# Optimization experiments

Hardware: AMD Instinct MI355X
Metric: run time of the kernel (lower is better)

## Reference

```python
import jax, jax.numpy as jnp
import numpy as np

C = 1024      # channels
K = 7         # kernel_size
G = 1         # groups (G>1 crashes in the original torch code; see notes)
GC = C // G   # group_channels
OFFSET_SCALE = 2.0
LN_EPS = 1e-5


def setup_inputs() -> dict:
    key = jax.random.key(0)
    ks = jax.random.split(key, 8)
    N, L = 4, 2048
    s = 1.0 / np.sqrt(C)
    x = jax.random.normal(ks[0], (N, L, C), jnp.float32)
    Wi = jax.random.normal(ks[1], (C, C), jnp.float32) * s
    bi = jnp.zeros((C,), jnp.float32)
    dw_w = jax.random.normal(ks[2], (C, 1, 3), jnp.float32) * 0.5   # depthwise conv kernel (O, I/g=1, W)
    dw_b = jnp.zeros((C,), jnp.float32)
    ln_g = jnp.ones((C,), jnp.float32)
    ln_b = jnp.zeros((C,), jnp.float32)
    Wo = jax.random.normal(ks[3], (G * K, C), jnp.float32) * 0.02   # offset head (nonzero to exercise gather)
    bo = jnp.zeros((G * K,), jnp.float32)
    Wm = jax.random.normal(ks[4], (G * K, C), jnp.float32) * 0.02   # mask head
    bm = jnp.zeros((G * K,), jnp.float32)
    Wout = jax.random.normal(ks[5], (C, C), jnp.float32) * s
    bout = jnp.zeros((C,), jnp.float32)
    return {"x": x, "Wi": Wi, "bi": bi, "dw_w": dw_w, "dw_b": dw_b,
            "ln_g": ln_g, "ln_b": ln_b, "Wo": Wo, "bo": bo,
            "Wm": Wm, "bm": bm, "Wout": Wout, "bout": bout}


def _forward(x, Wi, bi, dw_w, dw_b, ln_g, ln_b, Wo, bo, Wm, bm, Wout, bout):
    N, L, Cc = x.shape
    dt = x.dtype
    # input projection
    x_proj = x @ Wi.T + bi                                  # [N,L,C]
    # depthwise conv (k=3, pad=1, groups=C) -> LayerNorm(C) -> GELU(exact)
    y = jax.lax.conv_general_dilated(
        x.transpose(0, 2, 1), dw_w, window_strides=(1,), padding=((1, 1),),
        dimension_numbers=("NCH", "OIH", "NCH"), feature_group_count=Cc)
    x_dw = y.transpose(0, 2, 1) + dw_b                       # [N,L,C]
    mu = x_dw.mean(-1, keepdims=True)
    var = ((x_dw - mu) ** 2).mean(-1, keepdims=True)
    x_dw = (x_dw - mu) * jax.lax.rsqrt(var + LN_EPS) * ln_g + ln_b
    x_dw = jax.nn.gelu(x_dw, approximate=False)
    # dynamic offsets and sampling mask
    offsets = (x_dw @ Wo.T + bo).reshape(N, L, G, K) * OFFSET_SCALE
    mask = jax.nn.softmax((x_dw @ Wm.T + bm).reshape(N, L, G, K), axis=-1)
    mask = jnp.nan_to_num(mask, nan=0.0)
    # absolute sampling positions
    ref_off = jnp.linspace(-(K // 2), K // 2, K).astype(dt)          # [K]
    pos = jnp.arange(L, dtype=dt)[None, :, None, None]               # [1,L,1,1]
    abs_pos = pos + ref_off[None, None, None, :] + offsets           # [N,L,G,K]
    apc = jnp.clip(abs_pos, 0.0, L - 1)
    p_floor = jnp.clip(apc.astype(jnp.int32), 0, L - 1)
    p_ceil = jnp.clip(p_floor + 1, 0, L - 1)
    w_ceil = apc - p_floor.astype(dt)
    w_floor = 1.0 - w_ceil
    valid = jnp.logical_not((abs_pos < 0) | (abs_pos > L - 1)).astype(dt)
    w_floor = w_floor * valid
    w_ceil = w_ceil * valid
    # gather + bilinear blend (G=1: each sample index grabs the full C channels)
    idx_f = p_floor.reshape(N, -1)[:, :, None]                       # [N, L*G*K, 1]
    idx_c = p_ceil.reshape(N, -1)[:, :, None]
    v_floor = jnp.take_along_axis(x_proj, idx_f, axis=1).reshape(N, L, G, K, GC)
    v_ceil = jnp.take_along_axis(x_proj, idx_c, axis=1).reshape(N, L, G, K, GC)
    sampled = v_floor * w_floor[..., None] + v_ceil * w_ceil[..., None]
    out = (sampled * mask[..., None]).sum(axis=3).reshape(N, L, Cc)  # sum over K
    return out @ Wout.T + bout


def reference(x, Wi, bi, dw_w, dw_b, ln_g, ln_b, Wo, bo, Wm, bm, Wout, bout):
    return _forward(x, Wi, bi, dw_w, dw_b, ln_g, ln_b, Wo, bo, Wm, bm, Wout, bout)
```

## Files before the change

kernel.cpp:

```cpp
#include <hip/hip_runtime.h>
#include <hip/hip_bf16.h>
#include <cstdint>

#define C_DIM 1024
#define L_DIM 2048
#define N_DIM 4
#define M_DIM (N_DIM * L_DIM)

typedef __attribute__((ext_vector_type(8))) short frag8;
typedef __attribute__((ext_vector_type(4)))  float f32x4;
typedef __attribute__((ext_vector_type(16))) float f32x16;

__device__ __forceinline__ void gl_lds16(const void* g, void* l) {
  __builtin_amdgcn_global_load_lds((const __attribute__((address_space(1))) void*)g,
                                   (__attribute__((address_space(3))) void*)l,
                                   16, 0, 0);
}
__device__ __forceinline__ void store_out(float* Y, size_t idx, float v) { Y[idx] = v; }
__device__ __forceinline__ void store_out(__hip_bfloat16* Y, size_t idx, float v) {
  Y[idx] = __float2bfloat16(v);
}
__device__ __forceinline__ float4 ldbf4(const __hip_bfloat16* p) {
  union { short4 s; __hip_bfloat16 h[4]; } u; u.s = *(const short4*)p;
  return make_float4((float)u.h[0], (float)u.h[1], (float)u.h[2], (float)u.h[3]);
}
__device__ __forceinline__ void stbf4(__hip_bfloat16* p, float4 v) {
  union { short4 s; __hip_bfloat16 h[4]; } u;
  u.h[0] = __float2bfloat16(v.x); u.h[1] = __float2bfloat16(v.y);
  u.h[2] = __float2bfloat16(v.z); u.h[3] = __float2bfloat16(v.w);
  *(short4*)p = u.s;
}
__device__ __forceinline__ float gelu_fast(float t) {
  const float t3 = t * t * t;
  const float ns = -1.5957691216f * t - 0.0713548163f * t3;
  return t / (1.f + __expf(ns));
}

__global__ __launch_bounds__(256)
void cvt_f32_bf16(const float* __restrict__ in, __hip_bfloat16* __restrict__ out, int n8) {
  const int i = blockIdx.x * 256 + threadIdx.x;
  if (i >= n8) return;
  const float4 a = *(const float4*)(in + (size_t)i * 8);
  const float4 b = *(const float4*)(in + (size_t)i * 8 + 4);
  union { __hip_bfloat16 h[8]; int4 q; } u;
  u.h[0] = __float2bfloat16(a.x); u.h[1] = __float2bfloat16(a.y);
  u.h[2] = __float2bfloat16(a.z); u.h[3] = __float2bfloat16(a.w);
  u.h[4] = __float2bfloat16(b.x); u.h[5] = __float2bfloat16(b.y);
  u.h[6] = __float2bfloat16(b.z); u.h[7] = __float2bfloat16(b.w);
  *(int4*)(out + (size_t)i * 8) = u.q;
}

template <typename TY>
__global__ __launch_bounds__(256, 2)
void gemm_db(const __hip_bfloat16* __restrict__ X,
             const __hip_bfloat16* __restrict__ W,
             const float* __restrict__ bias,
             TY* __restrict__ Y, int M, int N, int K)
{
  __shared__ __hip_bfloat16 As[2][2][128 * 32];
  __shared__ __hip_bfloat16 Bs[2][2][128 * 32];
  const int tid  = threadIdx.x;
  const int lane = tid & 63;
  const int wave = tid >> 6;
  const int bm = blockIdx.x * 128;
  const int bn = blockIdx.y * 128;
  const int wr = (wave >> 1) * 64;
  const int wc = (wave & 1) * 64;
  const int srow  = tid >> 2;
  const int skoff = (tid & 3) * 8;

  const __hip_bfloat16* gA0 = X + (size_t)(bm + srow) * K + skoff;
  const __hip_bfloat16* gA1 = X + (size_t)(bm + 64 + srow) * K + skoff;
  const __hip_bfloat16* gB0 = W + (size_t)(bn + srow) * K + skoff;
  const __hip_bfloat16* gB1 = W + (size_t)(bn + 64 + srow) * K + skoff;

  f32x16 acc[2][2] = {};
  const int arow  = lane & 31;
  const int akoff = (lane >> 5) * 8;

#define STAGE(k0, buf)                                        \
  do {                                                        \
    gl_lds16(gA0 + (k0),      &As[buf][0][tid * 8]);          \
    gl_lds16(gA1 + (k0),      &As[buf][0][2048 + tid * 8]);   \
    gl_lds16(gA0 + (k0) + 32, &As[buf][1][tid * 8]);          \
    gl_lds16(gA1 + (k0) + 32, &As[buf][1][2048 + tid * 8]);   \
    gl_lds16(gB0 + (k0),      &Bs[buf][0][tid * 8]);          \
    gl_lds16(gB1 + (k0),      &Bs[buf][0][2048 + tid * 8]);   \
    gl_lds16(gB0 + (k0) + 32, &Bs[buf][1][tid * 8]);          \
    gl_lds16(gB1 + (k0) + 32, &Bs[buf][1][2048 + tid * 8]);   \
  } while (0)

  STAGE(0, 0);
  __syncthreads();
  const int iters = K / 64;
  for (int it = 0; it < iters; ++it) {
    const int cur = it & 1;
    if (it + 1 < iters) STAGE((it + 1) * 64, cur ^ 1);

#pragma unroll
    for (int p = 0; p < 2; ++p)
#pragma unroll
      for (int h = 0; h < 2; ++h) {
        const frag8 a0 = *(const frag8*)&As[cur][p][(wr + arow) * 32 + h * 16 + akoff];
        const frag8 a1 = *(const frag8*)&As[cur][p][(wr + 32 + arow) * 32 + h * 16 + akoff];
        const frag8 b0 = *(const frag8*)&Bs[cur][p][(wc + arow) * 32 + h * 16 + akoff];
        const frag8 b1 = *(const frag8*)&Bs[cur][p][(wc + 32 + arow) * 32 + h * 16 + akoff];
        acc[0][0] = __builtin_amdgcn_mfma_f32_32x32x16_bf16(a0, b0, acc[0][0], 0, 0, 0);
        acc[0][1] = __builtin_amdgcn_mfma_f32_32x32x16_bf16(a0, b1, acc[0][1], 0, 0, 0);
        acc[1][0] = __builtin_amdgcn_mfma_f32_32x32x16_bf16(a1, b0, acc[1][0], 0, 0, 0);
        acc[1][1] = __builtin_amdgcn_mfma_f32_32x32x16_bf16(a1, b1, acc[1][1], 0, 0, 0);
      }
    __syncthreads();
  }
#undef STAGE

#pragma unroll
  for (int i = 0; i < 2; i++)
#pragma unroll
    for (int j = 0; j < 2; j++) {
      const int col = bn + wc + j * 32 + (lane & 31);
      const float bv = bias[col];
#pragma unroll
      for (int r = 0; r < 16; r++) {
        const int row = bm + wr + i * 32 + (r & 3) + 8 * (r >> 2) + 4 * (lane >> 5);
        store_out(Y, (size_t)row * N + col, acc[i][j][r] + bv);
      }
    }
}

struct Ld8f { float4 a, b; };
struct Ld8b { int4 a; };
__device__ __forceinline__ Ld8f ld8(const float* p) {
  return { *(const float4*)p, *(const float4*)(p + 4) };
}
__device__ __forceinline__ Ld8b ld8(const __hip_bfloat16* p) { return { *(const int4*)p }; }
__device__ __forceinline__ void st8(__hip_bfloat16* l, const Ld8f& v) {
  union { __hip_bfloat16 h[8]; int4 q; } u;
  u.h[0] = __float2bfloat16(v.a.x); u.h[1] = __float2bfloat16(v.a.y);
  u.h[2] = __float2bfloat16(v.a.z); u.h[3] = __float2bfloat16(v.a.w);
  u.h[4] = __float2bfloat16(v.b.x); u.h[5] = __float2bfloat16(v.b.y);
  u.h[6] = __float2bfloat16(v.b.z); u.h[7] = __float2bfloat16(v.b.w);
  *(int4*)l = u.q;
}
__device__ __forceinline__ void st8(__hip_bfloat16* l, const Ld8b& v) { *(int4*)l = v.a; }

template <typename TX, typename TY>
__global__ __launch_bounds__(256, 2)
void gemm_nt(const TX* __restrict__ X, const float* __restrict__ W,
             const float* __restrict__ bias, TY* __restrict__ Y, int M, int N, int K)
{
  __shared__ __hip_bfloat16 As[128 * 32];
  __shared__ __hip_bfloat16 Bs[128 * 32];
  const int tid  = threadIdx.x;
  const int lane = tid & 63;
  const int wave = tid >> 6;
  const int bm = blockIdx.x * 128;
  const int bn = blockIdx.y * 128;
  const int wr = (wave >> 1) * 64;
  const int wc = (wave & 1) * 64;
  const int srow  = tid >> 2;
  const int skoff = (tid & 3) * 8;

  f32x4 acc[4][4] = {};
  const TX*    gA0 = X + (size_t)(bm + srow) * K + skoff;
  const TX*    gA1 = X + (size_t)(bm + 64 + srow) * K + skoff;
  const float* gB0 = W + (size_t)(bn + srow) * K + skoff;
  const float* gB1 = W + (size_t)(bn + 64 + srow) * K + skoff;
  const int arow  = lane & 15;
  const int akoff = (lane >> 4) * 8;

  for (int k0 = 0; k0 < K; k0 += 32) {
    const auto va0 = ld8(gA0 + k0);
    const auto va1 = ld8(gA1 + k0);
    const auto vb0 = ld8(gB0 + k0);
    const auto vb1 = ld8(gB1 + k0);
    __syncthreads();
    st8(&As[srow * 32 + skoff],        va0);
    st8(&As[(64 + srow) * 32 + skoff], va1);
    st8(&Bs[srow * 32 + skoff],        vb0);
    st8(&Bs[(64 + srow) * 32 + skoff], vb1);
    __syncthreads();

    frag8 a[4], b[4];
#pragma unroll
    for (int i = 0; i < 4; i++)
      a[i] = *(const frag8*)&As[(wr + i * 16 + arow) * 32 + akoff];
#pragma unroll
    for (int j = 0; j < 4; j++)
      b[j] = *(const frag8*)&Bs[(wc + j * 16 + arow) * 32 + akoff];
#pragma unroll
    for (int i = 0; i < 4; i++)
#pragma unroll
      for (int j = 0; j < 4; j++)
        acc[i][j] = __builtin_amdgcn_mfma_f32_16x16x32_bf16(a[i], b[j], acc[i][j], 0, 0, 0);
  }
#pragma unroll
  for (int i = 0; i < 4; i++)
#pragma unroll
    for (int j = 0; j < 4; j++) {
      const int col = bn + wc + j * 16 + (lane & 15);
      const float bv = bias[col];
#pragma unroll
      for (int r = 0; r < 4; r++) {
        const int row = bm + wr + i * 16 + (lane >> 4) * 4 + r;
        store_out(Y, (size_t)row * N + col, acc[i][j][r] + bv);
      }
    }
}

__global__ __launch_bounds__(256)
void mid_fused_v4(const float* __restrict__ x,
                  const float* __restrict__ dw_w, const float* __restrict__ dw_b,
                  const float* __restrict__ ln_g, const float* __restrict__ ln_b,
                  const float* __restrict__ Wo,   const float* __restrict__ bo,
                  const float* __restrict__ Wm,   const float* __restrict__ bmb,
                  const __hip_bfloat16* __restrict__ xp,
                  __hip_bfloat16* __restrict__ smp)
{
  const int b    = blockIdx.x;
  const int bs   = (b & 7) * 256 + (b >> 3);
  const int wid  = threadIdx.x >> 6;
  const int lane = threadIdx.x & 63;
  const int row  = bs * 4 + wid;
  const int l    = row & (L_DIM - 1);
  const int n    = row >> 11;

  const float* xr = x + (size_t)row * C_DIM;

  float4 v[4];
#pragma unroll
  for (int j = 0; j < 4; j++) {
    const int c4 = j * 256 + lane * 4;
    const float4 x0 = *(const float4*)(xr + c4);
    float4 xm = make_float4(0.f, 0.f, 0.f, 0.f);
    float4 xq = make_float4(0.f, 0.f, 0.f, 0.f);
    if (l > 0)         xm = *(const float4*)(xr + c4 - C_DIM);
    if (l < L_DIM - 1) xq = *(const float4*)(xr + c4 + C_DIM);
    const float4 w0 = *(const float4*)(dw_w + (size_t)c4 * 3);
    const float4 w1 = *(const float4*)(dw_w + (size_t)c4 * 3 + 4);
    const float4 w2 = *(const float4*)(dw_w + (size_t)c4 * 3 + 8);
    const float4 bb = *(const float4*)(dw_b + c4);
    v[j].x = xm.x * w0.x + x0.x * w0.y + xq.x * w0.z + bb.x;
    v[j].y = xm.y * w0.w + x0.y * w1.x + xq.y * w1.y + bb.y;
    v[j].z = xm.z * w1.z + x0.z * w1.w + xq.z * w2.x + bb.z;
    v[j].w = xm.w * w2.y + x0.w * w2.z + xq.w * w2.w + bb.w;
  }

  float s1 = 0.f, s2 = 0.f;
#pragma unroll
  for (int j = 0; j < 4; j++) {
    s1 += v[j].x + v[j].y + v[j].z + v[j].w;
    s2 += v[j].x * v[j].x + v[j].y * v[j].y + v[j].z * v[j].z + v[j].w * v[j].w;
  }
#pragma unroll
  for (int m = 1; m < 64; m <<= 1) { s1 += __shfl_xor(s1, m); s2 += __shfl_xor(s2, m); }
  const float mu   = s1 * (1.f / C_DIM);
  const float rstd = rsqrtf(s2 * (1.f / C_DIM) - mu * mu + 1e-5f);

  float4 g[4];
#pragma unroll
  for (int j = 0; j < 4; j++) {
    const int c4 = j * 256 + lane * 4;
    const float4 gg = *(const float4*)(ln_g + c4);
    const float4 bb = *(const float4*)(ln_b + c4);
    g[j].x = gelu_fast((v[j].x - mu) * rstd * gg.x + bb.x);
    g[j].y = gelu_fast((v[j].y - mu) * rstd * gg.y + bb.y);
    g[j].z = gelu_fast((v[j].z - mu) * rstd * gg.z + bb.z);
    g[j].w = gelu_fast((v[j].w - mu) * rstd * gg.w + bb.w);
  }

  float po[7] = {0,0,0,0,0,0,0}, pm[7] = {0,0,0,0,0,0,0};
#pragma unroll
  for (int k = 0; k < 7; k++) {
#pragma unroll
    for (int j = 0; j < 4; j++) {
      const int c4 = j * 256 + lane * 4;
      const float4 wo = *(const float4*)(Wo + (size_t)k * C_DIM + c4);
      const float4 wm = *(const float4*)(Wm + (size_t)k * C_DIM + c4);
      po[k] += g[j].x * wo.x + g[j].y * wo.y + g[j].z * wo.z + g[j].w * wo.w;
      pm[k] += g[j].x * wm.x + g[j].y * wm.y + g[j].z * wm.z + g[j].w * wm.w;
    }
  }
#pragma unroll
  for (int k = 0; k < 7; k++)
#pragma unroll
    for (int m = 1; m < 64; m <<= 1) {
      po[k] += __shfl_xor(po[k], m);
      pm[k] += __shfl_xor(pm[k], m);
    }

  float lg[7], mx = -1e30f;
#pragma unroll
  for (int k = 0; k < 7; k++) { lg[k] = pm[k] + bmb[k]; mx = fmaxf(mx, lg[k]); }
  float se = 0.f, e[7];
#pragma unroll
  for (int k = 0; k < 7; k++) { e[k] = __expf(lg[k] - mx); se += e[k]; }
  const float inv = 1.f / se;

  float wf[7], wcl[7]; int pf[7], pc[7];
#pragma unroll
  for (int k = 0; k < 7; k++) {
    const float msk = e[k] * inv;
    const float off = (po[k] + bo[k]) * 2.0f;
    const float ap  = (float)l + (float)(k - 3) + off;
    const float apc = fminf(fmaxf(ap, 0.f), (float)(L_DIM - 1));
    int f = (int)apc;
    int c = f + 1; if (c > L_DIM - 1) c = L_DIM - 1;
    const float w1  = apc - (float)f;
    const float val = (ap < 0.f || ap > (float)(L_DIM - 1)) ? 0.f : 1.f;
    wf[k]  = (1.f - w1) * val * msk;
    wcl[k] = w1 * val * msk;
    pf[k] = f; pc[k] = c;
  }

  const __hip_bfloat16* xpn = xp + ((size_t)n * L_DIM) * C_DIM;
  __hip_bfloat16* so = smp + (size_t)row * C_DIM;
#pragma unroll
  for (int j = 0; j < 4; j++) {
    const int c4 = j * 256 + lane * 4;
    float4 a = make_float4(0.f, 0.f, 0.f, 0.f);
#pragma unroll
    for (int k = 0; k < 7; k++) {
      const float4 vf = ldbf4(xpn + (size_t)pf[k] * C_DIM + c4);
      const float4 vc = ldbf4(xpn + (size_t)pc[k] * C_DIM + c4);
      a.x += wf[k] * vf.x + wcl[k] * vc.x;
      a.y += wf[k] * vf.y + wcl[k] * vc.y;
      a.z += wf[k] * vf.z + wcl[k] * vc.z;
      a.w += wf[k] * vf.w + wcl[k] * vc.w;
    }
    stbf4(so + c4, a);
  }
}

extern "C" void kernel_launch(void* const* d_in, const int* in_sizes, int n_in,
                              void* d_out, int out_size, void* d_ws, size_t ws_size,
                              hipStream_t stream)
{
  const float* x    = (const float*)d_in[0];
  const float* Wi   = (const float*)d_in[1];
  const float* bi   = (const float*)d_in[2];
  const float* dw_w = (const float*)d_in[3];
  const float* dw_b = (const float*)d_in[4];
  const float* ln_g = (const float*)d_in[5];
  const float* ln_b = (const float*)d_in[6];
  const float* Wo   = (const float*)d_in[7];
  const float* bo   = (const float*)d_in[8];
  const float* Wm   = (const float*)d_in[9];
  const float* bm   = (const float*)d_in[10];
  const float* Wout = (const float*)d_in[11];
  const float* bout = (const float*)d_in[12];
  float* out = (float*)d_out;

  const size_t XE = (size_t)M_DIM * C_DIM;
  const size_t WE = (size_t)C_DIM * C_DIM;
  char* wsb = (char*)d_ws;
  __hip_bfloat16* xp    = (__hip_bfloat16*)wsb;
  __hip_bfloat16* smp   = (__hip_bfloat16*)(wsb + XE * 2);
  __hip_bfloat16* Wib   = (__hip_bfloat16*)(wsb + XE * 4);
  __hip_bfloat16* Woutb = (__hip_bfloat16*)(wsb + XE * 4 + WE * 2);
  __hip_bfloat16* xbb   = (__hip_bfloat16*)(wsb + XE * 4 + WE * 4);

  const size_t need_w2   = XE * 4 + WE * 4;
  const size_t need_full = need_w2 + XE * 2;

  dim3 gg(M_DIM / 128, C_DIM / 128);

  if (ws_size >= need_full) {
    cvt_f32_bf16<<<(int)(XE / 8 / 256), 256, 0, stream>>>(x, xbb, (int)(XE / 8));
    cvt_f32_bf16<<<(int)(WE / 8 / 256), 256, 0, stream>>>(Wi, Wib, (int)(WE / 8));
    cvt_f32_bf16<<<(int)(WE / 8 / 256), 256, 0, stream>>>(Wout, Woutb, (int)(WE / 8));
    gemm_db<__hip_bfloat16><<<gg, 256, 0, stream>>>(xbb, Wib, bi, xp, M_DIM, C_DIM, C_DIM);
    mid_fused_v4<<<M_DIM / 4, 256, 0, stream>>>(x, dw_w, dw_b, ln_g, ln_b, Wo, bo, Wm, bm, xp, smp);
    gemm_db<float><<<gg, 256, 0, stream>>>(smp, Woutb, bout, out, M_DIM, C_DIM, C_DIM);
  } else if (ws_size >= need_w2) {
    cvt_f32_bf16<<<(int)(WE / 8 / 256), 256, 0, stream>>>(Wout, Woutb, (int)(WE / 8));
    gemm_nt<float, __hip_bfloat16><<<gg, 256, 0, stream>>>(x, Wi, bi, xp, M_DIM, C_DIM, C_DIM);
    mid_fused_v4<<<M_DIM / 4, 256, 0, stream>>>(x, dw_w, dw_b, ln_g, ln_b, Wo, bo, Wm, bm, xp, smp);
    gemm_db<float><<<gg, 256, 0, stream>>>(smp, Woutb, bout, out, M_DIM, C_DIM, C_DIM);
  } else {
    gemm_nt<float, __hip_bfloat16><<<gg, 256, 0, stream>>>(x, Wi, bi, xp, M_DIM, C_DIM, C_DIM);
    mid_fused_v4<<<M_DIM / 4, 256, 0, stream>>>(x, dw_w, dw_b, ln_g, ln_b, Wo, bo, Wm, bm, xp, smp);
    gemm_nt<__hip_bfloat16, float><<<gg, 256, 0, stream>>>(smp, Wout, bout, out, M_DIM, C_DIM, C_DIM);
  }
}
```

Before: 203.9 us.

## Fuse x bf16 conversion with conv/LN/GELU/offset heads; split gather into separate kernel

Adds a pre_fused kernel that reads x once and does three things: writes its bf16 copy, computes the depthwise conv, LayerNorm, GELU and offset/mask heads, and stores per-row bilinear coefficients and indices. A lightweight gather kernel then blends the projected rows using those coefficients. This removes the standalone x conversion pass and the second read of fp32 x in the mid kernel, at the cost of an extra launch and a small coefficient buffer. The new path runs only when the workspace is large enough to hold that buffer.

```diff
diff --git a/kernel.cpp b/kernel.cpp
--- a/kernel.cpp
+++ b/kernel.cpp
@@ -209,6 +209,171 @@
 }
 
 __global__ __launch_bounds__(256)
+void pre_fused(const float* __restrict__ x,
+               const float* __restrict__ dw_w, const float* __restrict__ dw_b,
+               const float* __restrict__ ln_g, const float* __restrict__ ln_b,
+               const float* __restrict__ Wo,   const float* __restrict__ bo,
+               const float* __restrict__ Wm,   const float* __restrict__ bmb,
+               __hip_bfloat16* __restrict__ xbb,
+               float* __restrict__ coef)
+{
+  const int b    = blockIdx.x;
+  const int bs   = (b & 7) * 256 + (b >> 3);
+  const int wid  = threadIdx.x >> 6;
+  const int lane = threadIdx.x & 63;
+  const int row  = bs * 4 + wid;
+  const int l    = row & (L_DIM - 1);
+
+  const float* xr = x + (size_t)row * C_DIM;
+  __hip_bfloat16* xbr = xbb + (size_t)row * C_DIM;
+
+  float4 v[4];
+#pragma unroll
+  for (int j = 0; j < 4; j++) {
+    const int c4 = j * 256 + lane * 4;
+    const float4 x0 = *(const float4*)(xr + c4);
+    stbf4(xbr + c4, x0);
+    float4 xm = make_float4(0.f, 0.f, 0.f, 0.f);
+    float4 xq = make_float4(0.f, 0.f, 0.f, 0.f);
+    if (l > 0)         xm = *(const float4*)(xr + c4 - C_DIM);
+    if (l < L_DIM - 1) xq = *(const float4*)(xr + c4 + C_DIM);
+    const float4 w0 = *(const float4*)(dw_w + (size_t)c4 * 3);
+    const float4 w1 = *(const float4*)(dw_w + (size_t)c4 * 3 + 4);
+    const float4 w2 = *(const float4*)(dw_w + (size_t)c4 * 3 + 8);
+    const float4 bb = *(const float4*)(dw_b + c4);
+    v[j].x = xm.x * w0.x + x0.x * w0.y + xq.x * w0.z + bb.x;
+    v[j].y = xm.y * w0.w + x0.y * w1.x + xq.y * w1.y + bb.y;
+    v[j].z = xm.z * w1.z + x0.z * w1.w + xq.z * w2.x + bb.z;
+    v[j].w = xm.w * w2.y + x0.w * w2.z + xq.w * w2.w + bb.w;
+  }
+
+  float s1 = 0.f, s2 = 0.f;
+#pragma unroll
+  for (int j = 0; j < 4; j++) {
+    s1 += v[j].x + v[j].y + v[j].z + v[j].w;
+    s2 += v[j].x * v[j].x + v[j].y * v[j].y + v[j].z * v[j].z + v[j].w * v[j].w;
+  }
+#pragma unroll
+  for (int m = 1; m < 64; m <<= 1) { s1 += __shfl_xor(s1, m); s2 += __shfl_xor(s2, m); }
+  const float mu   = s1 * (1.f / C_DIM);
+  const float rstd = rsqrtf(s2 * (1.f / C_DIM) - mu * mu + 1e-5f);
+
+  float4 g[4];
+#pragma unroll
+  for (int j = 0; j < 4; j++) {
+    const int c4 = j * 256 + lane * 4;
+    const float4 gg = *(const float4*)(ln_g + c4);
+    const float4 bb = *(const float4*)(ln_b + c4);
+    g[j].x = gelu_fast((v[j].x - mu) * rstd * gg.x + bb.x);
+    g[j].y = gelu_fast((v[j].y - mu) * rstd * gg.y + bb.y);
+    g[j].z = gelu_fast((v[j].z - mu) * rstd * gg.z + bb.z);
+    g[j].w = gelu_fast((v[j].w - mu) * rstd * gg.w + bb.w);
+  }
+
+  float po[7] = {0,0,0,0,0,0,0}, pm[7] = {0,0,0,0,0,0,0};
+#pragma unroll
+  for (int k = 0; k < 7; k++) {
+#pragma unroll
+    for (int j = 0; j < 4; j++) {
+      const int c4 = j * 256 + lane * 4;
+      const float4 wo = *(const float4*)(Wo + (size_t)k * C_DIM + c4);
+      const float4 wm = *(const float4*)(Wm + (size_t)k * C_DIM + c4);
+      po[k] += g[j].x * wo.x + g[j].y * wo.y + g[j].z * wo.z + g[j].w * wo.w;
+      pm[k] += g[j].x * wm.x + g[j].y * wm.y + g[j].z * wm.z + g[j].w * wm.w;
+    }
+  }
+#pragma unroll
+  for (int k = 0; k < 7; k++)
+#pragma unroll
+    for (int m = 1; m < 64; m <<= 1) {
+      po[k] += __shfl_xor(po[k], m);
+      pm[k] += __shfl_xor(pm[k], m);
+    }
+
+  float lg[7], mx = -1e30f;
+#pragma unroll
+  for (int k = 0; k < 7; k++) { lg[k] = pm[k] + bmb[k]; mx = fmaxf(mx, lg[k]); }
+  float se = 0.f, e[7];
+#pragma unroll
+  for (int k = 0; k < 7; k++) { e[k] = __expf(lg[k] - mx); se += e[k]; }
+  const float inv = 1.f / se;
+
+  if (lane == 0) {
+    float pk[32];
+#pragma unroll
+    for (int k = 0; k < 7; k++) {
+      const float msk = e[k] * inv;
+      const float off = (po[k] + bo[k]) * 2.0f;
+      const float ap  = (float)l + (float)(k - 3) + off;
+      const float apc = fminf(fmaxf(ap, 0.f), (float)(L_DIM - 1));
+      int f = (int)apc;
+      int c = f + 1; if (c > L_DIM - 1) c = L_DIM - 1;
+      const float w1  = apc - (float)f;
+      const float val = (ap < 0.f || ap > (float)(L_DIM - 1)) ? 0.f : 1.f;
+      pk[k]      = (1.f - w1) * val * msk;
+      pk[8 + k]  = w1 * val * msk;
+      pk[16 + k] = (float)f;
+      pk[24 + k] = (float)c;
+    }
+    pk[7] = pk[15] = pk[23] = pk[31] = 0.f;
+    float* cr = coef + (size_t)row * 32;
+#pragma unroll
+    for (int q = 0; q < 8; q++)
+      *(float4*)(cr + q * 4) = make_float4(pk[q*4], pk[q*4+1], pk[q*4+2], pk[q*4+3]);
+  }
+}
+
+__global__ __launch_bounds__(256)
+void gather_k(const float* __restrict__ coef,
+              const __hip_bfloat16* __restrict__ xp,
+              __hip_bfloat16* __restrict__ smp)
+{
+  const int b    = blockIdx.x;
+  const int bs   = (b & 7) * 256 + (b >> 3);
+  const int wid  = threadIdx.x >> 6;
+  const int lane = threadIdx.x & 63;
+  const int row  = bs * 4 + wid;
+  const int n    = row >> 11;
+
+  const float* cr = coef + (size_t)row * 32;
+  const float4 q0 = *(const float4*)(cr);
+  const float4 q1 = *(const float4*)(cr + 4);
+  const float4 q2 = *(const float4*)(cr + 8);
+  const float4 q3 = *(const float4*)(cr + 12);
+  const float4 q4 = *(const float4*)(cr + 16);
+  const float4 q5 = *(const float4*)(cr + 20);
+  const float4 q6 = *(const float4*)(cr + 24);
+  const float4 q7 = *(const float4*)(cr + 28);
+
+  const float wf[7] = {q0.x, q0.y, q0.z, q0.w, q1.x, q1.y, q1.z};
+  const float wc[7] = {q2.x, q2.y, q2.z, q2.w, q3.x, q3.y, q3.z};
+  const int   pf[7] = {(int)q4.x, (int)q4.y, (int)q4.z, (int)q4.w, (int)q5.x, (int)q5.y, (int)q5.z};
+  const int   pc[7] = {(int)q6.x, (int)q6.y, (int)q6.z, (int)q6.w, (int)q7.x, (int)q7.y, (int)q7.z};
+
+  const __hip_bfloat16* xpn = xp + ((size_t)n * L_DIM) * C_DIM;
+  __hip_bfloat16* so = smp + (size_t)row * C_DIM;
+
+#pragma unroll
+  for (int j = 0; j < 2; j++) {
+    const int c8 = j * 512 + lane * 8;
+    float a[8] = {0.f, 0.f, 0.f, 0.f, 0.f, 0.f, 0.f, 0.f};
+#pragma unroll
+    for (int k = 0; k < 7; k++) {
+      union { int4 q; __hip_bfloat16 h[8]; } uf, uc;
+      uf.q = *(const int4*)(xpn + (size_t)pf[k] * C_DIM + c8);
+      uc.q = *(const int4*)(xpn + (size_t)pc[k] * C_DIM + c8);
+#pragma unroll
+      for (int t = 0; t < 8; t++)
+        a[t] += wf[k] * (float)uf.h[t] + wc[k] * (float)uc.h[t];
+    }
+    union { int4 q; __hip_bfloat16 h[8]; } uo;
+#pragma unroll
+    for (int t = 0; t < 8; t++) uo.h[t] = __float2bfloat16(a[t]);
+    *(int4*)(so + c8) = uo.q;
+  }
+}
+
+__global__ __launch_bounds__(256)
 void mid_fused_v4(const float* __restrict__ x,
                   const float* __restrict__ dw_w, const float* __restrict__ dw_b,
                   const float* __restrict__ ln_g, const float* __restrict__ ln_b,
@@ -359,13 +524,22 @@
   __hip_bfloat16* Wib   = (__hip_bfloat16*)(wsb + XE * 4);
   __hip_bfloat16* Woutb = (__hip_bfloat16*)(wsb + XE * 4 + WE * 2);
   __hip_bfloat16* xbb   = (__hip_bfloat16*)(wsb + XE * 4 + WE * 4);
-
-  const size_t need_w2   = XE * 4 + WE * 4;
-  const size_t need_full = need_w2 + XE * 2;
+  float*          coef  = (float*)(wsb + XE * 4 + WE * 4 + XE * 2);
+
+  const size_t need_w2    = XE * 4 + WE * 4;
+  const size_t need_full  = need_w2 + XE * 2;
+  const size_t need_full2 = need_full + (size_t)M_DIM * 32 * 4;
 
   dim3 gg(M_DIM / 128, C_DIM / 128);
 
-  if (ws_size >= need_full) {
+  if (ws_size >= need_full2) {
+    cvt_f32_bf16<<<(int)(WE / 8 / 256), 256, 0, stream>>>(Wi, Wib, (int)(WE / 8));
+    cvt_f32_bf16<<<(int)(WE / 8 / 256), 256, 0, stream>>>(Wout, Woutb, (int)(WE / 8));
+    pre_fused<<<M_DIM / 4, 256, 0, stream>>>(x, dw_w, dw_b, ln_g, ln_b, Wo, bo, Wm, bm, xbb, coef);
+    gemm_db<__hip_bfloat16><<<gg, 256, 0, stream>>>(xbb, Wib, bi, xp, M_DIM, C_DIM, C_DIM);
+    gather_k<<<M_DIM / 4, 256, 0, stream>>>(coef, xp, smp);
+    gemm_db<float><<<gg, 256, 0, stream>>>(smp, Woutb, bout, out, M_DIM, C_DIM, C_DIM);
+  } else if (ws_size >= need_full) {
     cvt_f32_bf16<<<(int)(XE / 8 / 256), 256, 0, stream>>>(x, xbb, (int)(XE / 8));
     cvt_f32_bf16<<<(int)(WE / 8 / 256), 256, 0, stream>>>(Wi, Wib, (int)(WE / 8));
     cvt_f32_bf16<<<(int)(WE / 8 / 256), 256, 0, stream>>>(Wout, Woutb, (int)(WE / 8));
```

Result: no change. 207.2 us (+1.7%).
